# Kernel tuning notes

Measured on AMD Instinct MI355X. Metric: run time of the kernel, lower is better.

## Reference

```python
import jax, jax.numpy as jnp
import numpy as np

B = 32768
NPG = 15            # nodes per graph (5 segments * 3 nodes)
NSEG = 5
FEAT = 8
HID = 64
BIAS_SP = float(np.log(np.exp(1.0) - 1.0))  # biased_softplus_1.0 bias
SCALE_LB = 1e-4


def _edge_template():
    eg = []
    for s in range(NSEG):
        t = 3 * s
        eg += [(t, t + 1), (t + 1, t), (t, t + 2), (t + 2, t)]
    for s in range(NSEG - 1):
        eg += [(3 * s, 3 * s + 3), (3 * s + 3, 3 * s)]
    return np.asarray(eg, dtype=np.int64)  # [28, 2]


def setup_inputs() -> dict:
    key = jax.random.key(0)
    ks = jax.random.split(key, 16)
    N = B * NPG
    x = jax.random.normal(ks[0], (N, FEAT), dtype=jnp.float32)
    tmpl = _edge_template()
    offs = (np.arange(B, dtype=np.int64) * NPG)[:, None]          # [B,1]
    src = (tmpl[:, 0][None, :] + offs).ravel()
    dst = (tmpl[:, 1][None, :] + offs).ravel()
    edge_index = jnp.asarray(np.stack([src, dst]), dtype=jnp.int32)  # [2,E]
    sd = 0.05
    params = dict(
        Wt=jax.random.normal(ks[1], (FEAT, HID), jnp.float32) * sd,
        bt=jax.random.normal(ks[2], (HID,), jnp.float32) * sd,
        Wl=jax.random.normal(ks[3], (4, HID), jnp.float32) * sd,
        bl=jax.random.normal(ks[4], (HID,), jnp.float32) * sd,
        gc_Wroot=jax.random.normal(ks[5], (3, HID, HID), jnp.float32) * sd,
        gc_Wrel=jax.random.normal(ks[6], (3, HID, HID), jnp.float32) * sd,
        gc_b=jax.random.normal(ks[7], (3, HID), jnp.float32) * sd,
        leg_W=jax.random.normal(ks[8], (10, HID, 4), jnp.float32) * sd,
        leg_b=jax.random.normal(ks[9], (10, 4), jnp.float32) * sd,
        torso_W=jax.random.normal(ks[10], (4, HID, 4), jnp.float32) * sd,
        torso_b=jax.random.normal(ks[11], (4, 4), jnp.float32) * sd,
    )
    return dict(x=x, edge_index=edge_index, batch_size=B, **params)


def reference(x, edge_index, batch_size, Wt, bt, Wl, bl,
              gc_Wroot, gc_Wrel, gc_b, leg_W, leg_b, torso_W, torso_b):
    N = x.shape[0]
    npg = N // batch_size              # 15
    nseg = npg // 3                    # 5
    pos = jnp.arange(N) % npg
    is_torso = (pos % 3) == 0          # nodes 0,3,6,... within each graph

    # Per-type input encoders + tanh, merged by mask (original scatters into h)
    h_t = jnp.tanh(x @ Wt + bt)
    h_l = jnp.tanh(x[:, :4] @ Wl + bl)
    h = jnp.where(is_torso[:, None], h_t, h_l)        # [N, 64]

    src, dst = edge_index[0], edge_index[1]
    for i in range(3):
        agg = jax.ops.segment_sum(h[src], dst, num_segments=N)
        h = jnp.tanh(agg @ gc_Wrel[i] + gc_b[i] + h @ gc_Wroot[i])

    hp = h.reshape(batch_size, npg, HID)              # [B, 15, 64]

    leg_pos = jnp.array([p for p in range(1, npg) if p % 3 != 0])   # 10 legs
    torso_pos = jnp.array([3 * s for s in range(1, nseg)])          # 4 torsos

    leg_out = jnp.einsum('bnd,ndk->bnk', hp[:, leg_pos], leg_W) + leg_b      # [B,10,4]
    torso_out = jnp.einsum('bnd,ndk->bnk', hp[:, torso_pos], torso_W) + torso_b  # [B,4,4]

    # Blocks are emitted in node-position order 1..14 within each graph
    blocks = jnp.zeros((batch_size, npg - 1, 4), dtype=h.dtype)
    blocks = blocks.at[:, leg_pos - 1].set(leg_out)
    blocks = blocks.at[:, torso_pos - 1].set(torso_out)
    out = blocks.reshape(batch_size, 2 * (npg - 1), 2)               # [B,28,2]

    loc = out[..., 0]
    scale = jnp.maximum(jax.nn.softplus(out[..., 1] + BIAS_SP), SCALE_LB)
    return loc, scale
```

## Files before the change

kernel.cpp:

```cpp
#include <hip/hip_runtime.h>

#define NB 32768
#define GPB 8
#define THREADS 256
#define BIAS_SP 0.5413248546129181f

typedef __attribute__((ext_vector_type(8))) short bf16x8;
typedef __attribute__((ext_vector_type(4))) float f32x4;
typedef __attribute__((ext_vector_type(4))) unsigned int u32x4;

static __device__ __forceinline__ unsigned f2bfu(float f) {
    union { float f; unsigned u; } v; v.f = f;
    return (v.u + 0x8000u) >> 16;
}
static __device__ __forceinline__ unsigned f2bfu_hi(float f) {
    union { float f; unsigned u; } v; v.f = f;
    return (v.u + 0x8000u) & 0xFFFF0000u;
}
static __device__ __forceinline__ float lof(unsigned u) {
    union { unsigned u; float f; } v; v.u = u << 16; return v.f;
}
static __device__ __forceinline__ float hif(unsigned u) {
    union { unsigned u; float f; } v; v.u = u & 0xFFFF0000u; return v.f;
}
static __device__ __forceinline__ float fast_tanh(float xx) {
    float e = __expf(2.0f * xx);
    return 1.0f - 2.0f * __builtin_amdgcn_rcpf(e + 1.0f);
}

__global__ void setup_kernel(const float* __restrict__ Wroot, const float* __restrict__ Wrel,
                             const float* __restrict__ legW, const float* __restrict__ torW,
                             unsigned* __restrict__ wsw) {
    const int t = blockIdx.x * 256 + threadIdx.x;
    if (t < 3072) {
        const int i = t >> 10, rem = t & 1023, s = rem >> 8, tt = rem & 255;
        const int lane = tt & 63, ctl = tt >> 6;
        const int bcol = (ctl << 4) + (lane & 15);
        const int kb = ((s & 1) << 5) + ((lane >> 4) << 3);
        const float* M = ((s < 2) ? Wroot : Wrel) + i * 4096 + kb * 64 + bcol;
        u32x4 d;
        #pragma unroll
        for (int dd = 0; dd < 4; ++dd)
            d[dd] = f2bfu(M[(2 * dd) * 64]) | (f2bfu(M[(2 * dd + 1) * 64]) << 16);
        *(u32x4*)(wsw + t * 4) = d;
    } else if (t < 3520) {
        const int t2 = t - 3072, item = t2 >> 3, k8 = t2 & 7;
        const int p = (item >> 2) + 1, j = item & 3;
        const int p3 = (p * 11) >> 5;
        const int pm3 = p - p3 * 3;
        const float* src;
        if (pm3 == 0) src = torW + (p3 - 1) * 256 + j;
        else          src = legW + (2 * p3 + pm3 - 1) * 256 + j;
        u32x4 d;
        #pragma unroll
        for (int dd = 0; dd < 4; ++dd) {
            const int k = (k8 << 3) + 2 * dd;
            d[dd] = f2bfu(src[k * 4]) | (f2bfu(src[(k + 1) * 4]) << 16);
        }
        *(u32x4*)(wsw + 12288 + t2 * 4) = d;
    }
}

__global__ __launch_bounds__(THREADS, 4) void leg_main(
    const float* __restrict__ x,
    const float* __restrict__ Wt, const float* __restrict__ bt,
    const float* __restrict__ Wl, const float* __restrict__ bl,
    const float* __restrict__ gcb,
    const float* __restrict__ legB, const float* __restrict__ torB,
    const unsigned* __restrict__ wsw,
    float* __restrict__ out)
{
    __shared__ __align__(16) unsigned char smem[GPB * 4096];
    const int tid  = threadIdx.x;
    const int lane = tid & 63;
    const int ct   = tid >> 6;
    const int g0   = blockIdx.x * GPB;

    const int bcol = (ct << 4) + (lane & 15);
    const float cb0 = gcb[bcol], cb1 = gcb[64 + bcol], cb2 = gcb[128 + bcol];

    const int colb = ((lane >> 3) << 4) + ((lane & 7) << 1);
    const int row = lane & 15, kg = lane >> 4;
    const int row3 = (row * 11) >> 5;
    const int tors = row3 * 3;
    const int isT  = (row == tors);
    const int rowR = isT ? row : tors;
    const int voffA0 = row * 256 + (((kg ^ row) & 7) << 4);
    const int voffA2 = rowR * 256 + (((kg ^ rowR) & 7) << 4) + (isT ? 128 : 0);
    int voffC[4];
    #pragma unroll
    for (int r = 0; r < 4; ++r) {
        const int rr = (kg << 2) + r;
        voffC[r] = rr * 256 + (((((ct << 1) + ((lane >> 3) & 1)) ^ rr) & 7) << 4) + ((lane & 7) << 1);
    }

    const int half = lane >> 5;
    const int c2   = lane & 31;
    unsigned char* gbase = smem + ((ct << 1) + half) * 4096;
    const int aoff = (c2 & 3) << 2;
    int agg_ra[15];
    #pragma unroll
    for (int r = 0; r < 15; ++r)
        agg_ra[r] = r * 256 + ((((c2 >> 2) ^ r) & 7) << 4) + aoff;
    int agg_wa[5];
    #pragma unroll
    for (int i = 0; i < 5; ++i) {
        const int r = 3 * i;
        agg_wa[i] = r * 256 + 128 + ((((c2 >> 2) ^ r) & 7) << 4) + aoff;
    }
#define RD32(r)  (*(const unsigned*)(gbase + agg_ra[r]))
#define WR32(i, flo, fhi) *(unsigned*)(gbase + agg_wa[i]) = (f2bfu(flo) | f2bfu_hi(fhi))
#define AGG() do { \
    unsigned u[15]; \
    _Pragma("unroll") for (int r = 0; r < 15; ++r) u[r] = RD32(r); \
    float l3 = lof(u[3]), h3 = hif(u[3]), l6 = lof(u[6]), h6 = hif(u[6]), l9 = lof(u[9]), h9 = hif(u[9]); \
    WR32(0,  lof(u[1]) + lof(u[2]) + l3,              hif(u[1]) + hif(u[2]) + h3); \
    WR32(1,  lof(u[4]) + lof(u[5]) + lof(u[0]) + l6,  hif(u[4]) + hif(u[5]) + hif(u[0]) + h6); \
    WR32(2,  lof(u[7]) + lof(u[8]) + l3 + l9,         hif(u[7]) + hif(u[8]) + h3 + h9); \
    WR32(3,  lof(u[10]) + lof(u[11]) + l6 + lof(u[12]), hif(u[10]) + hif(u[11]) + h6 + hif(u[12])); \
    WR32(4,  lof(u[13]) + lof(u[14]) + l9,            hif(u[13]) + hif(u[14]) + h9); \
} while (0)

    float ewt[8], ewl[4];
    #pragma unroll
    for (int k = 0; k < 8; ++k) ewt[k] = Wt[(k << 6) + lane];
    #pragma unroll
    for (int k = 0; k < 4; ++k) ewl[k] = Wl[(k << 6) + lane];
    const float ebt = bt[lane], ebl = bl[lane];

    #pragma unroll
    for (int gs = 0; gs < 2; ++gs) {
        const int g = (ct << 1) + gs;
        const float4* xg = (const float4*)(x + (size_t)(g0 + g) * 120);
        unsigned char* sb = smem + g * 4096;
        #pragma unroll
        for (int p = 0; p < 15; ++p) {
            const float4 a0 = xg[p * 2];
            float acc;
            if (p % 3 == 0) {
                const float4 a1 = xg[p * 2 + 1];
                acc = ebt + a0.x * ewt[0] + a0.y * ewt[1] + a0.z * ewt[2] + a0.w * ewt[3]
                          + a1.x * ewt[4] + a1.y * ewt[5] + a1.z * ewt[6] + a1.w * ewt[7];
            } else {
                acc = ebl + a0.x * ewl[0] + a0.y * ewl[1] + a0.z * ewl[2] + a0.w * ewl[3];
            }
            *(unsigned short*)(sb + p * 256 + (colb ^ ((p & 7) << 4))) =
                (unsigned short)f2bfu(fast_tanh(acc));
        }
        *(unsigned short*)(sb + 15 * 256 + (colb ^ 0x70)) = 0;
        *(unsigned short*)(sb + 15 * 256 + 128 + (colb ^ 0x70)) = 0;
    }
    __syncthreads();
    AGG();
    __syncthreads();

    #pragma unroll
    for (int it = 0; it < 3; ++it) {
        bf16x8 bfr[4];
        #pragma unroll
        for (int s = 0; s < 4; ++s)
            bfr[s] = *(const bf16x8*)(wsw + ((it * 4 + s) * 256 + tid) * 4);
        const float cbi = (it == 0) ? cb0 : (it == 1) ? cb1 : cb2;
        f32x4 acc[GPB];
        #pragma unroll
        for (int g = 0; g < GPB; ++g) {
            const unsigned char* sg = smem + g * 4096;
            const bf16x8 a0 = *(const bf16x8*)(sg + voffA0);
            const bf16x8 a1 = *(const bf16x8*)(sg + (voffA0 ^ 0x40));
            const bf16x8 a2 = *(const bf16x8*)(sg + voffA2);
            const bf16x8 a3 = *(const bf16x8*)(sg + (voffA2 ^ 0x40));
            f32x4 c = { cbi, cbi, cbi, cbi };
            c = __builtin_amdgcn_mfma_f32_16x16x32_bf16(a0, bfr[0], c, 0, 0, 0);
            c = __builtin_amdgcn_mfma_f32_16x16x32_bf16(a1, bfr[1], c, 0, 0, 0);
            c = __builtin_amdgcn_mfma_f32_16x16x32_bf16(a2, bfr[2], c, 0, 0, 0);
            c = __builtin_amdgcn_mfma_f32_16x16x32_bf16(a3, bfr[3], c, 0, 0, 0);
            acc[g] = c;
        }
        __syncthreads();
        #pragma unroll
        for (int g = 0; g < GPB; ++g)
            #pragma unroll
            for (int r = 0; r < 4; ++r)
                *(unsigned short*)(smem + g * 4096 + voffC[r]) =
                    (unsigned short)f2bfu(fast_tanh(acc[g][r]));
        __syncthreads();
        if (it < 2) { AGG(); __syncthreads(); }
    }

    if (lane < 56) {
        const int p = (lane >> 2) + 1, j = lane & 3;
        const int p3 = (p * 11) >> 5;
        const int pm3 = p - p3 * 3;
        float bias;
        if (pm3 == 0) bias = torB[((p3 - 1) << 2) + j];
        else          bias = legB[(((p3 << 1) + pm3 - 1) << 2) + j];
        const unsigned* wp = wsw + 12288 + (lane << 5);
        const int ps = (p & 7) << 4;
        #pragma unroll
        for (int gs = 0; gs < 2; ++gs) {
            const int g = (ct << 1) + gs;
            const unsigned char* hb = smem + g * 4096 + p * 256;
            float acc = 0.f;
            #pragma unroll
            for (int k8 = 0; k8 < 8; ++k8) {
                const u32x4 hv = *(const u32x4*)(hb + (ps ^ (k8 << 4)));
                const u32x4 wv = *(const u32x4*)(wp + (k8 << 2));
                #pragma unroll
                for (int dd = 0; dd < 4; ++dd) {
                    acc = __builtin_fmaf(lof(hv[dd]), lof(wv[dd]), acc);
                    acc = __builtin_fmaf(hif(hv[dd]), hif(wv[dd]), acc);
                }
            }
            acc += bias;
            const int mloc = ((p - 1) << 1) + (j >> 1);
            const size_t ob = (size_t)(g0 + g) * 28 + mloc;
            if ((j & 1) == 0) {
                out[ob] = acc;
            } else {
                const float z = acc + BIAS_SP;
                const float sp = (z > 15.f) ? z : __logf(1.f + __expf(z));
                out[(size_t)NB * 28 + ob] = fmaxf(sp, 1e-4f);
            }
        }
    }
}

extern "C" void kernel_launch(void* const* d_in, const int* in_sizes, int n_in,
                              void* d_out, int out_size, void* d_ws, size_t ws_size,
                              hipStream_t stream) {
    (void)in_sizes; (void)n_in; (void)out_size; (void)ws_size;
    const float* x     = (const float*)d_in[0];
    const float* Wt    = (const float*)d_in[3];
    const float* bt    = (const float*)d_in[4];
    const float* Wl    = (const float*)d_in[5];
    const float* bl    = (const float*)d_in[6];
    const float* Wroot = (const float*)d_in[7];
    const float* Wrel  = (const float*)d_in[8];
    const float* gcb   = (const float*)d_in[9];
    const float* legW  = (const float*)d_in[10];
    const float* legB  = (const float*)d_in[11];
    const float* torW  = (const float*)d_in[12];
    const float* torB  = (const float*)d_in[13];
    unsigned* wsw = (unsigned*)d_ws;
    setup_kernel<<<14, 256, 0, stream>>>(Wroot, Wrel, legW, torW, wsw);
    leg_main<<<NB / GPB, 256, 0, stream>>>(x, Wt, bt, Wl, bl, gcb, legB, torB, wsw,
                                           (float*)d_out);
}
```

Measured before the change: 79.45 us.

## Compute input encoders with one bf16 MFMA per graph and use packed bf16 conversion

The per-type input encoders (torso 8-dim, leg 4-dim, plus biases) now run as a single 16x16x32 bf16 MFMA per graph. Masked x rows are combined with a weight matrix prepacked in the setup kernel, with constant-1 slots carrying the biases, and the result is written through the shared epilogue. Scalar bf16 rounding is replaced by the hardware v_cvt_pk_bf16_f32 instruction in the aggregation and epilogue. The intent is to remove scalar FMA work and redundant x loads from the encoder stage. In exchange, x and the encoder weights are quantized to bf16 before the multiply, which lowers precision compared with the fp32 path.

```diff
diff --git a/kernel.cpp b/kernel.cpp
--- a/kernel.cpp
+++ b/kernel.cpp
@@ -13,10 +13,6 @@
     union { float f; unsigned u; } v; v.f = f;
     return (v.u + 0x8000u) >> 16;
 }
-static __device__ __forceinline__ unsigned f2bfu_hi(float f) {
-    union { float f; unsigned u; } v; v.f = f;
-    return (v.u + 0x8000u) & 0xFFFF0000u;
-}
 static __device__ __forceinline__ float lof(unsigned u) {
     union { unsigned u; float f; } v; v.u = u << 16; return v.f;
 }
@@ -27,9 +23,12 @@
     float e = __expf(2.0f * xx);
     return 1.0f - 2.0f * __builtin_amdgcn_rcpf(e + 1.0f);
 }
+#define CVTPK(d, a, b) asm("v_cvt_pk_bf16_f32 %0, %1, %2" : "=v"(d) : "v"(a), "v"(b))
 
 __global__ void setup_kernel(const float* __restrict__ Wroot, const float* __restrict__ Wrel,
                              const float* __restrict__ legW, const float* __restrict__ torW,
+                             const float* __restrict__ Wt, const float* __restrict__ bt,
+                             const float* __restrict__ Wl, const float* __restrict__ bl,
                              unsigned* __restrict__ wsw) {
     const int t = blockIdx.x * 256 + threadIdx.x;
     if (t < 3072) {
@@ -58,13 +57,30 @@
             d[dd] = f2bfu(src[k * 4]) | (f2bfu(src[(k + 1) * 4]) << 16);
         }
         *(u32x4*)(wsw + 12288 + t2 * 4) = d;
+    } else if (t < 3776) {
+        const int t3 = t - 3520;
+        const int lane = t3 & 63, ctl = t3 >> 6;
+        const int col = (ctl << 4) + (lane & 15);
+        const int kg = lane >> 4;
+        auto encval = [&](int k) -> float {
+            if (k < 8)   return Wt[k * 64 + col];
+            if (k < 12)  return Wl[(k - 8) * 64 + col];
+            if (k == 12) return bt[col];
+            if (k == 13) return bl[col];
+            return 0.f;
+        };
+        u32x4 d;
+        #pragma unroll
+        for (int dd = 0; dd < 4; ++dd) {
+            const int k0 = kg * 8 + 2 * dd;
+            d[dd] = f2bfu(encval(k0)) | (f2bfu(encval(k0 + 1)) << 16);
+        }
+        *(u32x4*)(wsw + 14080 + t3 * 4) = d;
     }
 }
 
 __global__ __launch_bounds__(THREADS, 4) void leg_main(
     const float* __restrict__ x,
-    const float* __restrict__ Wt, const float* __restrict__ bt,
-    const float* __restrict__ Wl, const float* __restrict__ bl,
     const float* __restrict__ gcb,
     const float* __restrict__ legB, const float* __restrict__ torB,
     const unsigned* __restrict__ wsw,
@@ -79,14 +95,15 @@
     const int bcol = (ct << 4) + (lane & 15);
     const float cb0 = gcb[bcol], cb1 = gcb[64 + bcol], cb2 = gcb[128 + bcol];
 
-    const int colb = ((lane >> 3) << 4) + ((lane & 7) << 1);
     const int row = lane & 15, kg = lane >> 4;
     const int row3 = (row * 11) >> 5;
     const int tors = row3 * 3;
     const int isT  = (row == tors);
     const int rowR = isT ? row : tors;
-    const int voffA0 = row * 256 + (((kg ^ row) & 7) << 4);
-    const int voffA2 = rowR * 256 + (((kg ^ rowR) & 7) << 4) + (isT ? 128 : 0);
+    const int voffA0  = row * 256 + (((kg ^ row) & 7) << 4);
+    const int voffA1  = voffA0 ^ 0x40;
+    const int voffA2  = rowR * 256 + (((kg ^ rowR) & 7) << 4) + (isT ? 128 : 0);
+    const int voffA3  = voffA2 ^ 0x40;
     int voffC[4];
     #pragma unroll
     for (int r = 0; r < 4; ++r) {
@@ -94,9 +111,8 @@
         voffC[r] = rr * 256 + (((((ct << 1) + ((lane >> 3) & 1)) ^ rr) & 7) << 4) + ((lane & 7) << 1);
     }
 
-    const int half = lane >> 5;
-    const int c2   = lane & 31;
-    unsigned char* gbase = smem + ((ct << 1) + half) * 4096;
+    const int c2 = lane & 31;
+    unsigned char* gbase = smem + ((ct << 1) + (lane >> 5)) * 4096;
     const int aoff = (c2 & 3) << 2;
     int agg_ra[15];
     #pragma unroll
@@ -109,7 +125,8 @@
         agg_wa[i] = r * 256 + 128 + ((((c2 >> 2) ^ r) & 7) << 4) + aoff;
     }
 #define RD32(r)  (*(const unsigned*)(gbase + agg_ra[r]))
-#define WR32(i, flo, fhi) *(unsigned*)(gbase + agg_wa[i]) = (f2bfu(flo) | f2bfu_hi(fhi))
+#define WR32(i, flo, fhi) do { unsigned _w; CVTPK(_w, flo, fhi); \
+    *(unsigned*)(gbase + agg_wa[i]) = _w; } while (0)
 #define AGG() do { \
     unsigned u[15]; \
     _Pragma("unroll") for (int r = 0; r < 15; ++r) u[r] = RD32(r); \
@@ -120,36 +137,39 @@
     WR32(3,  lof(u[10]) + lof(u[11]) + l6 + lof(u[12]), hif(u[10]) + hif(u[11]) + h6 + hif(u[12])); \
     WR32(4,  lof(u[13]) + lof(u[14]) + l9,            hif(u[13]) + hif(u[14]) + h9); \
 } while (0)
-
-    float ewt[8], ewl[4];
-    #pragma unroll
-    for (int k = 0; k < 8; ++k) ewt[k] = Wt[(k << 6) + lane];
-    #pragma unroll
-    for (int k = 0; k < 4; ++k) ewl[k] = Wl[(k << 6) + lane];
-    const float ebt = bt[lane], ebl = bl[lane];
-
-    #pragma unroll
-    for (int gs = 0; gs < 2; ++gs) {
-        const int g = (ct << 1) + gs;
-        const float4* xg = (const float4*)(x + (size_t)(g0 + g) * 120);
-        unsigned char* sb = smem + g * 4096;
-        #pragma unroll
-        for (int p = 0; p < 15; ++p) {
-            const float4 a0 = xg[p * 2];
-            float acc;
-            if (p % 3 == 0) {
-                const float4 a1 = xg[p * 2 + 1];
-                acc = ebt + a0.x * ewt[0] + a0.y * ewt[1] + a0.z * ewt[2] + a0.w * ewt[3]
-                          + a1.x * ewt[4] + a1.y * ewt[5] + a1.z * ewt[6] + a1.w * ewt[7];
-            } else {
-                acc = ebl + a0.x * ewl[0] + a0.y * ewl[1] + a0.z * ewl[2] + a0.w * ewl[3];
-            }
-            *(unsigned short*)(sb + p * 256 + (colb ^ ((p & 7) << 4))) =
-                (unsigned short)f2bfu(fast_tanh(acc));
-        }
-        *(unsigned short*)(sb + 15 * 256 + (colb ^ 0x70)) = 0;
-        *(unsigned short*)(sb + 15 * 256 + 128 + (colb ^ 0x70)) = 0;
-    }
+#define EPI() do { \
+    _Pragma("unroll") for (int g = 0; g < GPB; ++g) { \
+        _Pragma("unroll") for (int r = 0; r < 4; ++r) { \
+            const float tv = fast_tanh(acc[g][r]); \
+            unsigned uu; CVTPK(uu, tv, tv); \
+            *(unsigned short*)(smem + g * 4096 + voffC[r]) = (unsigned short)uu; \
+        } } } while (0)
+
+    const unsigned mT = (isT && row < 15) ? 0xFFFFFFFFu : 0u;
+    const unsigned mL = isT ? 0u : 0xFFFFFFFFu;
+    const unsigned m01 = (kg == 0) ? mT : ((kg == 1) ? mL : 0u);
+    const unsigned m45 = (kg == 0) ? mT : 0u;
+    const unsigned c1213 = (kg == 1) ? ((mT ? 0x3F80u : 0u) | (mL ? 0x3F800000u : 0u)) : 0u;
+    const int rowc = (row < 15) ? row : 0;
+    const bf16x8 bfrE = *(const bf16x8*)(wsw + 14080 + tid * 4);
+
+    f32x4 acc[GPB];
+    #pragma unroll
+    for (int g = 0; g < GPB; ++g) {
+        const float4* xr = (const float4*)x + ((size_t)(g0 + g) * 15 + rowc) * 2;
+        const float4 x0 = xr[0], x1 = xr[1];
+        unsigned a01, a23, a45, a67;
+        CVTPK(a01, x0.x, x0.y); CVTPK(a23, x0.z, x0.w);
+        CVTPK(a45, x1.x, x1.y); CVTPK(a67, x1.z, x1.w);
+        union { u32x4 u; bf16x8 b; } af;
+        af.u[0] = a01 & m01;
+        af.u[1] = a23 & m01;
+        af.u[2] = (a45 & m45) | c1213;
+        af.u[3] = a67 & m45;
+        const f32x4 z = { 0.f, 0.f, 0.f, 0.f };
+        acc[g] = __builtin_amdgcn_mfma_f32_16x16x32_bf16(af.b, bfrE, z, 0, 0, 0);
+    }
+    EPI();
     __syncthreads();
     AGG();
     __syncthreads();
@@ -161,14 +181,13 @@
         for (int s = 0; s < 4; ++s)
             bfr[s] = *(const bf16x8*)(wsw + ((it * 4 + s) * 256 + tid) * 4);
         const float cbi = (it == 0) ? cb0 : (it == 1) ? cb1 : cb2;
-        f32x4 acc[GPB];
         #pragma unroll
         for (int g = 0; g < GPB; ++g) {
             const unsigned char* sg = smem + g * 4096;
             const bf16x8 a0 = *(const bf16x8*)(sg + voffA0);
-            const bf16x8 a1 = *(const bf16x8*)(sg + (voffA0 ^ 0x40));
+            const bf16x8 a1 = *(const bf16x8*)(sg + voffA1);
             const bf16x8 a2 = *(const bf16x8*)(sg + voffA2);
-            const bf16x8 a3 = *(const bf16x8*)(sg + (voffA2 ^ 0x40));
+            const bf16x8 a3 = *(const bf16x8*)(sg + voffA3);
             f32x4 c = { cbi, cbi, cbi, cbi };
             c = __builtin_amdgcn_mfma_f32_16x16x32_bf16(a0, bfr[0], c, 0, 0, 0);
             c = __builtin_amdgcn_mfma_f32_16x16x32_bf16(a1, bfr[1], c, 0, 0, 0);
@@ -177,12 +196,7 @@
             acc[g] = c;
         }
         __syncthreads();
-        #pragma unroll
-        for (int g = 0; g < GPB; ++g)
-            #pragma unroll
-            for (int r = 0; r < 4; ++r)
-                *(unsigned short*)(smem + g * 4096 + voffC[r]) =
-                    (unsigned short)f2bfu(fast_tanh(acc[g][r]));
+        EPI();
         __syncthreads();
         if (it < 2) { AGG(); __syncthreads(); }
     }
@@ -200,24 +214,24 @@
         for (int gs = 0; gs < 2; ++gs) {
             const int g = (ct << 1) + gs;
             const unsigned char* hb = smem + g * 4096 + p * 256;
-            float acc = 0.f;
+            float acch = 0.f;
             #pragma unroll
             for (int k8 = 0; k8 < 8; ++k8) {
                 const u32x4 hv = *(const u32x4*)(hb + (ps ^ (k8 << 4)));
                 const u32x4 wv = *(const u32x4*)(wp + (k8 << 2));
                 #pragma unroll
                 for (int dd = 0; dd < 4; ++dd) {
-                    acc = __builtin_fmaf(lof(hv[dd]), lof(wv[dd]), acc);
-                    acc = __builtin_fmaf(hif(hv[dd]), hif(wv[dd]), acc);
+                    acch = __builtin_fmaf(lof(hv[dd]), lof(wv[dd]), acch);
+                    acch = __builtin_fmaf(hif(hv[dd]), hif(wv[dd]), acch);
                 }
             }
-            acc += bias;
+            acch += bias;
             const int mloc = ((p - 1) << 1) + (j >> 1);
             const size_t ob = (size_t)(g0 + g) * 28 + mloc;
             if ((j & 1) == 0) {
-                out[ob] = acc;
+                out[ob] = acch;
             } else {
-                const float z = acc + BIAS_SP;
+                const float z = acch + BIAS_SP;
                 const float sp = (z > 15.f) ? z : __logf(1.f + __expf(z));
                 out[(size_t)NB * 28 + ob] = fmaxf(sp, 1e-4f);
             }
@@ -242,7 +256,6 @@
     const float* torW  = (const float*)d_in[12];
     const float* torB  = (const float*)d_in[13];
     unsigned* wsw = (unsigned*)d_ws;
-    setup_kernel<<<14, 256, 0, stream>>>(Wroot, Wrel, legW, torW, wsw);
-    leg_main<<<NB / GPB, 256, 0, stream>>>(x, Wt, bt, Wl, bl, gcb, legB, torB, wsw,
-                                           (float*)d_out);
-}
+    setup_kernel<<<15, 256, 0, stream>>>(Wroot, Wrel, legW, torW, Wt, bt, Wl, bl, wsw);
+    leg_main<<<NB / GPB, 256, 0, stream>>>(x, gcb, legB, torB, wsw, (float*)d_out);
+}
```

Result: no change. 78.73 us (-0.9%).
